# Optimization experiments

Measured on AMD Instinct MI355X. Metric: run time of the kernel, lower is better.

Reference implementation:

```python
import jax, jax.numpy as jnp
import numpy as np

N, C, B, NPG, M, E = 131072, 128, 64, 2048, 64, 1048576
LN_EPS = 1e-5


def setup_inputs() -> dict:
    key = jax.random.key(0)
    ks = jax.random.split(key, 8)
    h = jax.random.normal(ks[0], (N, C), dtype=jnp.float32)
    edge_index = jax.random.randint(ks[1], (2, E), 0, N, dtype=jnp.int32)
    U = jax.random.normal(ks[2], (B, NPG, M), dtype=jnp.float32)
    W = jax.random.normal(ks[3], (M, C, C), dtype=jnp.float32) * 0.02
    lin_w = jax.random.normal(ks[4], (C, C), dtype=jnp.float32) * (1.0 / np.sqrt(C))
    lin_b = jax.random.normal(ks[5], (C,), dtype=jnp.float32) * 0.01
    ln_g = jnp.ones((C,), dtype=jnp.float32)
    ln_beta = jnp.zeros((C,), dtype=jnp.float32)
    return {"h": h, "U": U, "W": W, "lin_w": lin_w, "lin_b": lin_b,
            "ln_g": ln_g, "ln_beta": ln_beta, "edge_index": edge_index}


def _gfno_block(h, U, W, lin_w, lin_b, ln_g, ln_beta, edge_index):
    n_nodes, c = h.shape
    b, npg, m_avail = U.shape
    m = min(m_avail, W.shape[0])
    Um = U[:, :, :m]                      # [B, n, m]
    Wm = W[:m]                            # [m, C, C]
    # Block-diagonal spectral conv (equal-sized graphs -> batched einsum)
    hb = h.reshape(b, npg, c)             # [B, n, C]
    h_hat = jnp.einsum('bnm,bnc->bmc', Um, hb)        # U^T h per graph
    out_hat = jnp.einsum('bmc,mco->bmo', h_hat, Wm)   # per-mode mixing
    spec = jnp.einsum('bnm,bmo->bno', Um, out_hat).reshape(n_nodes, c)
    # Local scatter-mean aggregation
    src, dst = edge_index[0], edge_index[1]
    agg = jax.ops.segment_sum(h[src], dst, num_segments=n_nodes)   # [N, C]
    deg = jax.ops.segment_sum(jnp.ones((src.shape[0],), h.dtype), dst,
                              num_segments=n_nodes)
    deg = jnp.maximum(deg, 1.0)[:, None]
    local = (agg / deg) @ lin_w.T + lin_b
    # Residual + LayerNorm + GELU (exact, erf-based as torch default)
    x = h + spec + local
    mu = jnp.mean(x, axis=-1, keepdims=True)
    var = jnp.mean(jnp.square(x - mu), axis=-1, keepdims=True)
    xn = (x - mu) * jax.lax.rsqrt(var + LN_EPS) * ln_g + ln_beta
    return jax.nn.gelu(xn, approximate=False)


def reference(h, U, W, lin_w, lin_b, ln_g, ln_beta, edge_index):
    return _gfno_block(h, U, W, lin_w, lin_b, ln_g, ln_beta, edge_index)
```

## Files before the change

kernel.cpp:

```cpp
#include <hip/hip_runtime.h>
#include <math.h>

#define NN   131072
#define CN   128
#define BN   64
#define NPGN 2048
#define MN   64
#define EN   1048576

typedef unsigned short u16;
typedef unsigned int   u32;
typedef __attribute__((ext_vector_type(8))) short short8;
typedef __attribute__((ext_vector_type(4))) float f32x4;

__device__ __forceinline__ float bf2f(u16 u){ return __uint_as_float(((u32)u)<<16); }
__device__ __forceinline__ u16 f2bf(float f){
  u32 x = __float_as_uint(f);
  return (u16)((x + 0x7fffu + ((x>>16)&1u)) >> 16);
}

__global__ void k_count(const int* __restrict__ dst, int* __restrict__ deg){
  int e = blockIdx.x*256 + threadIdx.x;
  atomicAdd(&deg[dst[e]], 1);
}

__global__ void k_scan1(const int* __restrict__ deg, int* __restrict__ rowst, int* __restrict__ bsum){
  __shared__ int s[512];
  const int t = threadIdx.x;
  const int i = blockIdx.x*512 + t;
  int v = deg[i];
  s[t] = v;
  __syncthreads();
  for (int off=1; off<512; off<<=1){
    int a = (t>=off) ? s[t-off] : 0;
    __syncthreads();
    s[t] += a;
    __syncthreads();
  }
  rowst[i] = s[t] - v;
  if (t==511) bsum[blockIdx.x] = s[511];
}

__global__ void k_scan2(const int* __restrict__ bsum, int* __restrict__ bofs){
  __shared__ int s[256];
  const int t = threadIdx.x;
  int v = bsum[t];
  s[t] = v;
  __syncthreads();
  for (int off=1; off<256; off<<=1){
    int a = (t>=off) ? s[t-off] : 0;
    __syncthreads();
    s[t] += a;
    __syncthreads();
  }
  bofs[t] = s[t] - v;
}

__global__ void k_scan3(int* __restrict__ rowst, const int* __restrict__ bofs){
  int i = blockIdx.x*256 + threadIdx.x;
  rowst[i] += bofs[i>>9];
}

__global__ void k_fill(const int* __restrict__ src, const int* __restrict__ dst,
                       const int* __restrict__ rowst, int* __restrict__ cursor,
                       int* __restrict__ csr){
  int e = blockIdx.x*256 + threadIdx.x;
  int d = dst[e];
  int p = atomicAdd(&cursor[d], 1);
  csr[rowst[d] + p] = src[e];
}

__global__ void k_prepw(const float* __restrict__ lin_w, u16* __restrict__ wsw){
  int tid = blockIdx.x*256 + threadIdx.x;
  int g = tid >> 6, L = tid & 63;
  int ct = g >> 2, ks = g & 3;
  int o = L & 15, q = L >> 4;
  const float* srcp = lin_w + (ct*16+o)*CN + ks*32 + q*8;
  u16 tmp[8];
  #pragma unroll
  for (int j=0;j<8;++j) tmp[j] = f2bf(srcp[j]);
  *(uint4*)(wsw + (size_t)tid*8) = *(const uint4*)tmp;
}

__global__ void k_prepWT(const float* __restrict__ W, u16* __restrict__ WT16){
  __shared__ u16 st[128*132];
  const int t = threadIdx.x;
  const int m = blockIdx.x;
  const float* Wm = W + (size_t)m*CN*CN;
  #pragma unroll
  for (int it=0; it<16; ++it){
    int flat = (it*256 + t)*4;
    int c = flat >> 7, o = flat & 127;
    float4 v = *(const float4*)(Wm + flat);
    st[(o+0)*132 + c] = f2bf(v.x);
    st[(o+1)*132 + c] = f2bf(v.y);
    st[(o+2)*132 + c] = f2bf(v.z);
    st[(o+3)*132 + c] = f2bf(v.w);
  }
  __syncthreads();
  u16* dstm = WT16 + (size_t)m*CN*CN;
  #pragma unroll
  for (int it=0; it<8; ++it){
    int oidx = (it*256 + t)*8;
    int o = oidx >> 7, c = oidx & 127;
    uint4 v = *(const uint4*)&st[o*132 + c];
    *(uint4*)(dstm + (size_t)o*CN + c) = v;
  }
}

__global__ void k_prep_h(const float* __restrict__ h, u16* __restrict__ h16, u16* __restrict__ ht16){
  __shared__ u16 st[CN*72];
  const int t = threadIdx.x;
  const int b = blockIdx.x >> 5;
  const int n0 = (blockIdx.x & 31)*64;
  const float* srcb = h + ((size_t)b*NPGN + n0)*CN;
  u16* natb = h16 + ((size_t)b*NPGN + n0)*CN;
  #pragma unroll
  for (int j=0;j<8;++j){
    int fidx = (j*256+t)*4;
    int r = fidx>>7, c = fidx&127;
    float4 v = *(const float4*)(srcb + fidx);
    u16 q0=f2bf(v.x), q1=f2bf(v.y), q2=f2bf(v.z), q3=f2bf(v.w);
    ushort4 nv; nv.x=q0; nv.y=q1; nv.z=q2; nv.w=q3;
    *(ushort4*)(natb + fidx) = nv;
    st[(c+0)*72 + r] = q0; st[(c+1)*72 + r] = q1;
    st[(c+2)*72 + r] = q2; st[(c+3)*72 + r] = q3;
  }
  __syncthreads();
  #pragma unroll
  for (int j=0;j<4;++j){
    int oidx = (j*256+t)*8;
    int c = oidx>>6, nn = oidx&63;
    uint4 v = *(const uint4*)&st[c*72 + nn];
    *(uint4*)(ht16 + ((size_t)b*CN + c)*NPGN + n0 + nn) = v;
  }
}

__global__ void k_prep_U(const float* __restrict__ U, u16* __restrict__ U16, u16* __restrict__ Ut16){
  __shared__ u16 st2[MN*136];
  const int t = threadIdx.x;
  const int b = blockIdx.x >> 4;
  const int n0 = (blockIdx.x & 15)*128;
  const float* srcb = U + ((size_t)b*NPGN + n0)*MN;
  u16* natb = U16 + ((size_t)b*NPGN + n0)*MN;
  #pragma unroll
  for (int j=0;j<8;++j){
    int fidx = (j*256+t)*4;
    int r = fidx>>6, mm = fidx&63;
    float4 v = *(const float4*)(srcb + fidx);
    u16 q0=f2bf(v.x), q1=f2bf(v.y), q2=f2bf(v.z), q3=f2bf(v.w);
    ushort4 nv; nv.x=q0; nv.y=q1; nv.z=q2; nv.w=q3;
    *(ushort4*)(natb + fidx) = nv;
    st2[(mm+0)*136 + r] = q0; st2[(mm+1)*136 + r] = q1;
    st2[(mm+2)*136 + r] = q2; st2[(mm+3)*136 + r] = q3;
  }
  __syncthreads();
  #pragma unroll
  for (int j=0;j<4;++j){
    int oidx = (j*256+t)*8;
    int mm = oidx>>7, nn = oidx&127;
    uint4 v = *(const uint4*)&st2[mm*136 + nn];
    *(uint4*)(Ut16 + ((size_t)b*MN + mm)*NPGN + n0 + nn) = v;
  }
}

__global__ __launch_bounds__(256) void k_hhat(const u16* __restrict__ Ut16,
                                              const u16* __restrict__ ht16,
                                              float* __restrict__ hp){
  const int t = threadIdx.x;
  const int L = t & 63, w = t >> 6;
  const int b = blockIdx.x >> 3, q = blockIdx.x & 7;
  const int lo = L & 15, qd = (L >> 4) << 3;
  f32x4 acc[8] = {};
  const u16* Arow  = Ut16 + ((size_t)(b*MN + w*16 + lo))*NPGN + q*256 + qd;
  const u16* Bbase = ht16 + ((size_t)(b*CN + lo))*NPGN + q*256 + qd;
  #pragma unroll
  for (int ks=0; ks<8; ++ks){
    short8 af = *(const short8*)(Arow + ks*32);
    #pragma unroll
    for (int ct=0; ct<8; ++ct){
      short8 bf = *(const short8*)(Bbase + (size_t)ct*16*NPGN + ks*32);
      acc[ct] = __builtin_amdgcn_mfma_f32_16x16x32_bf16(af, bf, acc[ct], 0, 0, 0);
    }
  }
  const int rb = w*16 + ((L>>4)<<2);
  float* dstb = hp + ((size_t)q*BN + b)*MN*CN;
  #pragma unroll
  for (int ct=0; ct<8; ++ct)
    #pragma unroll
    for (int r=0; r<4; ++r)
      dstb[(size_t)(rb+r)*CN + ct*16 + lo] = acc[ct][r];
}

__global__ __launch_bounds__(256) void k_ohat(const float* __restrict__ hp,
                                              const u16* __restrict__ WT16,
                                              u16* __restrict__ ohatT){
  __shared__ u16 shHi[16*132];
  __shared__ u16 shLo[16*132];
  const int t = threadIdx.x;
  const int m  = blockIdx.x >> 2;
  const int bq = blockIdx.x & 3;

  {
    const int bl = t >> 4;
    const int c0 = (t & 15) * 8;
    const size_t S = (size_t)BN*MN*CN;
    const float* base = hp + ((size_t)(bq*16 + bl)*MN + m)*CN + c0;
    float a[8] = {0,0,0,0,0,0,0,0};
    #pragma unroll
    for (int q=0; q<8; ++q){
      float4 v0 = *(const float4*)(base + q*S);
      float4 v1 = *(const float4*)(base + q*S + 4);
      a[0]+=v0.x; a[1]+=v0.y; a[2]+=v0.z; a[3]+=v0.w;
      a[4]+=v1.x; a[5]+=v1.y; a[6]+=v1.z; a[7]+=v1.w;
    }
    u16 hi[8], lo[8];
    #pragma unroll
    for (int j=0;j<8;++j){
      hi[j] = f2bf(a[j]);
      lo[j] = f2bf(a[j] - bf2f(hi[j]));
    }
    *(uint4*)&shHi[bl*132 + c0] = *(const uint4*)hi;
    *(uint4*)&shLo[bl*132 + c0] = *(const uint4*)lo;
  }
  __syncthreads();

  const int L = t & 63, w = t >> 6;
  const int lo16 = L & 15, qd = (L >> 4) << 3;
  const u16* WTm = WT16 + (size_t)m*CN*CN;
  f32x4 acc[2] = {};
  #pragma unroll
  for (int ks=0; ks<4; ++ks){
    short8 ah = *(const short8*)&shHi[lo16*132 + ks*32 + qd];
    short8 al = *(const short8*)&shLo[lo16*132 + ks*32 + qd];
    #pragma unroll
    for (int ot=0; ot<2; ++ot){
      short8 bf = *(const short8*)(WTm + (size_t)(w*32 + ot*16 + lo16)*CN + ks*32 + qd);
      acc[ot] = __builtin_amdgcn_mfma_f32_16x16x32_bf16(ah, bf, acc[ot], 0, 0, 0);
      acc[ot] = __builtin_amdgcn_mfma_f32_16x16x32_bf16(al, bf, acc[ot], 0, 0, 0);
    }
  }
  const int rb = (L>>4)<<2;
  #pragma unroll
  for (int ot=0; ot<2; ++ot){
    #pragma unroll
    for (int r=0; r<4; ++r){
      int b = bq*16 + rb + r;
      int o = w*32 + ot*16 + lo16;
      ohatT[((size_t)b*CN + o)*MN + m] = f2bf(acc[ot][r]);
    }
  }
}

__global__ __launch_bounds__(256) void k_spec(const u16* __restrict__ U16,
                                              const u16* __restrict__ ohatT,
                                              u16* __restrict__ spec16){
  const int t = threadIdx.x;
  const int L = t & 63, w = t >> 6;
  const int b = blockIdx.x >> 4;
  const int n0 = (blockIdx.x & 15)*128;
  const int lo = L & 15, qd = (L >> 4) << 3;
  f32x4 acc[2][8] = {};
  const u16* Abase = U16  + ((size_t)(b*NPGN + n0 + w*32 + lo))*MN + qd;
  const u16* Bbase = ohatT + ((size_t)(b*CN + lo))*MN + qd;
  #pragma unroll
  for (int ks=0; ks<2; ++ks){
    short8 a0 = *(const short8*)(Abase + ks*32);
    short8 a1 = *(const short8*)(Abase + (size_t)16*MN + ks*32);
    #pragma unroll
    for (int ot=0; ot<8; ++ot){
      short8 bf = *(const short8*)(Bbase + (size_t)ot*16*MN + ks*32);
      acc[0][ot] = __builtin_amdgcn_mfma_f32_16x16x32_bf16(a0, bf, acc[0][ot], 0, 0, 0);
      acc[1][ot] = __builtin_amdgcn_mfma_f32_16x16x32_bf16(a1, bf, acc[1][ot], 0, 0, 0);
    }
  }
  const int rb = (L>>4)<<2;
  #pragma unroll
  for (int i=0;i<2;++i){
    u16* dstb = spec16 + ((size_t)(b*NPGN + n0 + w*32 + i*16 + rb))*CN + lo;
    #pragma unroll
    for (int ot=0; ot<8; ++ot)
      #pragma unroll
      for (int r=0; r<4; ++r)
        dstb[(size_t)r*CN + ot*16] = f2bf(acc[i][ot][r]);
  }
}

__device__ __forceinline__ void unp_add(float* a, uint4 p){
  a[0]+=bf2f((u16)(p.x&0xffffu)); a[1]+=bf2f((u16)(p.x>>16));
  a[2]+=bf2f((u16)(p.y&0xffffu)); a[3]+=bf2f((u16)(p.y>>16));
  a[4]+=bf2f((u16)(p.z&0xffffu)); a[5]+=bf2f((u16)(p.z>>16));
  a[6]+=bf2f((u16)(p.w&0xffffu)); a[7]+=bf2f((u16)(p.w>>16));
}

__global__ __launch_bounds__(256,8) void k_localep(
    const u16* __restrict__ h16, const u16* __restrict__ spec16,
    const u16* __restrict__ wsw,
    const int* __restrict__ rowst, const int* __restrict__ deg, const int* __restrict__ csr,
    const float* __restrict__ lin_b, const float* __restrict__ ln_g,
    const float* __restrict__ ln_beta, float* __restrict__ out){
  __shared__ u16 sv[32*136];
  __shared__ u16 sx16[32*132];
  const int t = threadIdx.x;
  const int w = t>>6, lane = t&63;
  const size_t n0 = (size_t)blockIdx.x*32;

  {
    const int g   = lane >> 4;
    const int c16 = lane & 15;
    #pragma unroll
    for (int p=0; p<4; ++p){
      const int iA = p*8 + w;
      const int iB = p*8 + 4 + w;
      const int nA = (int)n0 + iA, nB = (int)n0 + iB;
      const int rsA = rowst[nA], dgA = deg[nA];
      const int rsB = rowst[nB], dgB = deg[nB];
      const int reA = rsA + dgA, reB = rsB + dgB;
      int eA = rsA + g, eB = rsB + g;
      float accA[8] = {0.f,0.f,0.f,0.f,0.f,0.f,0.f,0.f};
      float accB[8] = {0.f,0.f,0.f,0.f,0.f,0.f,0.f,0.f};
      while (eA < reA || eB < reB){
        const bool vA0 = eA   < reA, vA1 = eA+4 < reA;
        const bool vB0 = eB   < reB, vB1 = eB+4 < reB;
        int sA0 = vA0 ? csr[eA]   : 0;
        int sA1 = vA1 ? csr[eA+4] : 0;
        int sB0 = vB0 ? csr[eB]   : 0;
        int sB1 = vB1 ? csr[eB+4] : 0;
        uint4 qA0 = {0u,0u,0u,0u}, qA1 = {0u,0u,0u,0u};
        uint4 qB0 = {0u,0u,0u,0u}, qB1 = {0u,0u,0u,0u};
        if (vA0) qA0 = *(const uint4*)(h16 + (size_t)sA0*CN + c16*8);
        if (vA1) qA1 = *(const uint4*)(h16 + (size_t)sA1*CN + c16*8);
        if (vB0) qB0 = *(const uint4*)(h16 + (size_t)sB0*CN + c16*8);
        if (vB1) qB1 = *(const uint4*)(h16 + (size_t)sB1*CN + c16*8);
        unp_add(accA, qA0); unp_add(accA, qA1);
        unp_add(accB, qB0); unp_add(accB, qB1);
        eA += 8; eB += 8;
      }
      #pragma unroll
      for (int j=0;j<8;++j){
        accA[j] += __shfl_xor(accA[j],16); accA[j] += __shfl_xor(accA[j],32);
        accB[j] += __shfl_xor(accB[j],16); accB[j] += __shfl_xor(accB[j],32);
      }
      const float invA = 1.0f / fmaxf((float)dgA, 1.0f);
      const float invB = 1.0f / fmaxf((float)dgB, 1.0f);
      if (g==0){
        u16 ta[8], tb[8];
        #pragma unroll
        for (int j=0;j<8;++j){ ta[j]=f2bf(accA[j]*invA); tb[j]=f2bf(accB[j]*invB); }
        *(uint4*)&sv[iA*136 + c16*8] = *(const uint4*)ta;
        *(uint4*)&sv[iB*136 + c16*8] = *(const uint4*)tb;
      }
    }
  }
  __syncthreads();

  const int rt = w&1, cb = w>>1;
  f32x4 acc[4] = {};
  #pragma unroll
  for (int ks=0; ks<4; ++ks){
    short8 af = *(const short8*)&sv[(rt*16 + (lane&15))*136 + ks*32 + ((lane>>4)<<3)];
    #pragma unroll
    for (int c4=0; c4<4; ++c4){
      const short8 bf = *(const short8*)(wsw + ((size_t)((cb*4+c4)*4+ks)*64 + lane)*8);
      acc[c4] = __builtin_amdgcn_mfma_f32_16x16x32_bf16(af, bf, acc[c4], 0, 0, 0);
    }
  }
  #pragma unroll
  for (int c4=0; c4<4; ++c4){
    int col = cb*64 + c4*16 + (lane&15);
    int rb = rt*16 + ((lane>>4)<<2);
    #pragma unroll
    for (int r=0; r<4; ++r) sx16[(rb+r)*132 + col] = f2bf(acc[c4][r]);
  }
  __syncthreads();

  float2 lb    = *(const float2*)(lin_b  + 2*lane);
  float2 lg    = *(const float2*)(ln_g   + 2*lane);
  float2 lbe   = *(const float2*)(ln_beta+ 2*lane);
  for (int r=0; r<8; ++r){
    int i = r*4 + w;
    size_t base = (n0 + i)*CN + 2*lane;
    u32 hA = *(const u32*)(h16 + base);
    u32 sA = *(const u32*)(spec16 + base);
    u32 lA = *(const u32*)&sx16[i*132 + 2*lane];
    float x0 = bf2f((u16)(hA&0xffffu)) + bf2f((u16)(sA&0xffffu)) + bf2f((u16)(lA&0xffffu)) + lb.x;
    float x1 = bf2f((u16)(hA>>16))     + bf2f((u16)(sA>>16))     + bf2f((u16)(lA>>16))     + lb.y;
    float s  = x0 + x1;
    float ss = fmaf(x0,x0, x1*x1);
    #pragma unroll
    for (int d=1; d<64; d<<=1){ s += __shfl_xor(s,d); ss += __shfl_xor(ss,d); }
    float mu  = s*(1.0f/128.0f);
    float var = ss*(1.0f/128.0f) - mu*mu;
    float rstd = rsqrtf(var + 1e-5f);
    float xn0 = (x0-mu)*rstd*lg.x + lbe.x;
    float xn1 = (x1-mu)*rstd*lg.y + lbe.y;
    float2 st;
    st.x = 0.5f*xn0*(1.0f + erff(xn0*0.70710678118654752f));
    st.y = 0.5f*xn1*(1.0f + erff(xn1*0.70710678118654752f));
    *(float2*)(out + base) = st;
  }
}

extern "C" void kernel_launch(void* const* d_in, const int* in_sizes, int n_in,
                              void* d_out, int out_size, void* d_ws, size_t ws_size,
                              hipStream_t stream) {
  const float* h      = (const float*)d_in[0];
  const float* U      = (const float*)d_in[1];
  const float* W      = (const float*)d_in[2];
  const float* lin_w  = (const float*)d_in[3];
  const float* lin_b  = (const float*)d_in[4];
  const float* ln_g   = (const float*)d_in[5];
  const float* ln_b2  = (const float*)d_in[6];
  const int* ei       = (const int*)d_in[7];
  const int* src = ei;
  const int* dst = ei + EN;
  float* out = (float*)d_out;

  char* wp = (char*)d_ws;
  float* hp     = (float*)wp; wp += (size_t)8*BN*MN*CN*sizeof(float);
  u16*   ohatT  = (u16*)wp;   wp += (size_t)BN*CN*MN*sizeof(u16);
  u16*   h16    = (u16*)wp;   wp += (size_t)NN*CN*sizeof(u16);
  u16*   ht16   = (u16*)wp;   wp += (size_t)BN*CN*NPGN*sizeof(u16);
  u16*   U16b   = (u16*)wp;   wp += (size_t)BN*NPGN*MN*sizeof(u16);
  u16*   Ut16   = (u16*)wp;   wp += (size_t)BN*MN*NPGN*sizeof(u16);
  u16*   spec16 = (u16*)wp;   wp += (size_t)NN*CN*sizeof(u16);
  u16*   wsw    = (u16*)wp;   wp += (size_t)CN*CN*sizeof(u16);
  u16*   WT16   = (u16*)wp;   wp += (size_t)MN*CN*CN*sizeof(u16);
  int*   deg    = (int*)wp;   wp += (size_t)NN*sizeof(int);
  int*   rowst  = (int*)wp;   wp += (size_t)NN*sizeof(int);
  int*   cursor = (int*)wp;   wp += (size_t)NN*sizeof(int);
  int*   csr    = (int*)wp;   wp += (size_t)EN*sizeof(int);
  int*   bsum   = (int*)wp;   wp += 512*sizeof(int);
  int*   bofs   = (int*)wp;   wp += 512*sizeof(int);

  hipMemsetAsync(deg,    0, (size_t)NN*sizeof(int), stream);
  hipMemsetAsync(cursor, 0, (size_t)NN*sizeof(int), stream);

  k_count<<<EN/256, 256, 0, stream>>>(dst, deg);
  k_scan1<<<NN/512, 512, 0, stream>>>(deg, rowst, bsum);
  k_scan2<<<1, 256, 0, stream>>>(bsum, bofs);
  k_scan3<<<NN/256, 256, 0, stream>>>(rowst, bofs);
  k_fill<<<EN/256, 256, 0, stream>>>(src, dst, rowst, cursor, csr);

  k_prepw<<<8, 256, 0, stream>>>(lin_w, wsw);
  k_prepWT<<<MN, 256, 0, stream>>>(W, WT16);
  k_prep_h<<<BN*32, 256, 0, stream>>>(h, h16, ht16);
  k_prep_U<<<BN*16, 256, 0, stream>>>(U, U16b, Ut16);

  k_hhat<<<BN*8, 256, 0, stream>>>(Ut16, ht16, hp);
  k_ohat<<<MN*4, 256, 0, stream>>>(hp, WT16, ohatT);
  k_spec<<<BN*16, 256, 0, stream>>>(U16b, ohatT, spec16);

  k_localep<<<NN/32, 256, 0, stream>>>(h16, spec16, wsw, rowst, deg, csr,
                                       lin_b, ln_g, ln_b2, out);
}
```

Measured before the change: 408.9 us.

## Fuse spectral back-projection GEMM into local epilogue kernel

Removes the separate k_spec kernel and computes the U·ohat product inside k_localep, accumulating into the same MFMA accumulators as the local linear layer. This avoids writing and re-reading the bf16 spec intermediate (about 32 MB of traffic) and saves one launch. In exchange, each block re-reads its ohatT slice and U rows, and the launch bound drops from 8 to 6 waves per SIMD to leave room for more registers. The spec term is now rounded to bf16 together with the local term instead of separately.

New measurement: 401.5 us. No clear change (-1.8%).

```diff
diff --git a/kernel.cpp b/kernel.cpp
--- a/kernel.cpp
+++ b/kernel.cpp
@@ -252,40 +252,6 @@
   }
 }
 
-__global__ __launch_bounds__(256) void k_spec(const u16* __restrict__ U16,
-                                              const u16* __restrict__ ohatT,
-                                              u16* __restrict__ spec16){
-  const int t = threadIdx.x;
-  const int L = t & 63, w = t >> 6;
-  const int b = blockIdx.x >> 4;
-  const int n0 = (blockIdx.x & 15)*128;
-  const int lo = L & 15, qd = (L >> 4) << 3;
-  f32x4 acc[2][8] = {};
-  const u16* Abase = U16  + ((size_t)(b*NPGN + n0 + w*32 + lo))*MN + qd;
-  const u16* Bbase = ohatT + ((size_t)(b*CN + lo))*MN + qd;
-  #pragma unroll
-  for (int ks=0; ks<2; ++ks){
-    short8 a0 = *(const short8*)(Abase + ks*32);
-    short8 a1 = *(const short8*)(Abase + (size_t)16*MN + ks*32);
-    #pragma unroll
-    for (int ot=0; ot<8; ++ot){
-      short8 bf = *(const short8*)(Bbase + (size_t)ot*16*MN + ks*32);
-      acc[0][ot] = __builtin_amdgcn_mfma_f32_16x16x32_bf16(a0, bf, acc[0][ot], 0, 0, 0);
-      acc[1][ot] = __builtin_amdgcn_mfma_f32_16x16x32_bf16(a1, bf, acc[1][ot], 0, 0, 0);
-    }
-  }
-  const int rb = (L>>4)<<2;
-  #pragma unroll
-  for (int i=0;i<2;++i){
-    u16* dstb = spec16 + ((size_t)(b*NPGN + n0 + w*32 + i*16 + rb))*CN + lo;
-    #pragma unroll
-    for (int ot=0; ot<8; ++ot)
-      #pragma unroll
-      for (int r=0; r<4; ++r)
-        dstb[(size_t)r*CN + ot*16] = f2bf(acc[i][ot][r]);
-  }
-}
-
 __device__ __forceinline__ void unp_add(float* a, uint4 p){
   a[0]+=bf2f((u16)(p.x&0xffffu)); a[1]+=bf2f((u16)(p.x>>16));
   a[2]+=bf2f((u16)(p.y&0xffffu)); a[3]+=bf2f((u16)(p.y>>16));
@@ -293,9 +259,9 @@
   a[6]+=bf2f((u16)(p.w&0xffffu)); a[7]+=bf2f((u16)(p.w>>16));
 }
 
-__global__ __launch_bounds__(256,8) void k_localep(
-    const u16* __restrict__ h16, const u16* __restrict__ spec16,
-    const u16* __restrict__ wsw,
+__global__ __launch_bounds__(256,6) void k_localep(
+    const u16* __restrict__ h16, const u16* __restrict__ U16,
+    const u16* __restrict__ ohatT, const u16* __restrict__ wsw,
     const int* __restrict__ rowst, const int* __restrict__ deg, const int* __restrict__ csr,
     const float* __restrict__ lin_b, const float* __restrict__ ln_g,
     const float* __restrict__ ln_beta, float* __restrict__ out){
@@ -355,19 +321,34 @@
   __syncthreads();
 
   const int rt = w&1, cb = w>>1;
+  const int lo16 = lane & 15, qd = (lane>>4)<<3;
   f32x4 acc[4] = {};
   #pragma unroll
   for (int ks=0; ks<4; ++ks){
-    short8 af = *(const short8*)&sv[(rt*16 + (lane&15))*136 + ks*32 + ((lane>>4)<<3)];
+    short8 af = *(const short8*)&sv[(rt*16 + lo16)*136 + ks*32 + qd];
     #pragma unroll
     for (int c4=0; c4<4; ++c4){
       const short8 bf = *(const short8*)(wsw + ((size_t)((cb*4+c4)*4+ks)*64 + lane)*8);
       acc[c4] = __builtin_amdgcn_mfma_f32_16x16x32_bf16(af, bf, acc[c4], 0, 0, 0);
     }
   }
+  {
+    const int b = (int)(n0 >> 11);
+    const u16* Au = U16  + ((size_t)(n0 + rt*16 + lo16))*MN + qd;
+    const u16* Bu = ohatT + ((size_t)(b*CN + cb*64 + lo16))*MN + qd;
+    #pragma unroll
+    for (int ks=0; ks<2; ++ks){
+      short8 af = *(const short8*)(Au + ks*32);
+      #pragma unroll
+      for (int c4=0; c4<4; ++c4){
+        short8 bf = *(const short8*)(Bu + (size_t)c4*16*MN + ks*32);
+        acc[c4] = __builtin_amdgcn_mfma_f32_16x16x32_bf16(af, bf, acc[c4], 0, 0, 0);
+      }
+    }
+  }
   #pragma unroll
   for (int c4=0; c4<4; ++c4){
-    int col = cb*64 + c4*16 + (lane&15);
+    int col = cb*64 + c4*16 + lo16;
     int rb = rt*16 + ((lane>>4)<<2);
     #pragma unroll
     for (int r=0; r<4; ++r) sx16[(rb+r)*132 + col] = f2bf(acc[c4][r]);
@@ -381,10 +362,9 @@
     int i = r*4 + w;
     size_t base = (n0 + i)*CN + 2*lane;
     u32 hA = *(const u32*)(h16 + base);
-    u32 sA = *(const u32*)(spec16 + base);
     u32 lA = *(const u32*)&sx16[i*132 + 2*lane];
-    float x0 = bf2f((u16)(hA&0xffffu)) + bf2f((u16)(sA&0xffffu)) + bf2f((u16)(lA&0xffffu)) + lb.x;
-    float x1 = bf2f((u16)(hA>>16))     + bf2f((u16)(sA>>16))     + bf2f((u16)(lA>>16))     + lb.y;
+    float x0 = bf2f((u16)(hA&0xffffu)) + bf2f((u16)(lA&0xffffu)) + lb.x;
+    float x1 = bf2f((u16)(hA>>16))     + bf2f((u16)(lA>>16))     + lb.y;
     float s  = x0 + x1;
     float ss = fmaf(x0,x0, x1*x1);
     #pragma unroll
@@ -423,7 +403,6 @@
   u16*   ht16   = (u16*)wp;   wp += (size_t)BN*CN*NPGN*sizeof(u16);
   u16*   U16b   = (u16*)wp;   wp += (size_t)BN*NPGN*MN*sizeof(u16);
   u16*   Ut16   = (u16*)wp;   wp += (size_t)BN*MN*NPGN*sizeof(u16);
-  u16*   spec16 = (u16*)wp;   wp += (size_t)NN*CN*sizeof(u16);
   u16*   wsw    = (u16*)wp;   wp += (size_t)CN*CN*sizeof(u16);
   u16*   WT16   = (u16*)wp;   wp += (size_t)MN*CN*CN*sizeof(u16);
   int*   deg    = (int*)wp;   wp += (size_t)NN*sizeof(int);
@@ -449,8 +428,7 @@
 
   k_hhat<<<BN*8, 256, 0, stream>>>(Ut16, ht16, hp);
   k_ohat<<<MN*4, 256, 0, stream>>>(hp, WT16, ohatT);
-  k_spec<<<BN*16, 256, 0, stream>>>(U16b, ohatT, spec16);
-
-  k_localep<<<NN/32, 256, 0, stream>>>(h16, spec16, wsw, rowst, deg, csr,
+
+  k_localep<<<NN/32, 256, 0, stream>>>(h16, U16b, ohatT, wsw, rowst, deg, csr,
                                        lin_b, ln_g, ln_b2, out);
 }
```
